# Kernel optimization log

Hardware: AMD Instinct MI355X
Metric: run time of the kernel (lower is better)

## Reference

```python
import jax, jax.numpy as jnp
import numpy as np

B, L, D, H = 2, 2048, 2048, 16
HD = D // H          # head dim = 128
R = int(HD * 0.25)   # rotary ndims = 32
SCALE = HD ** -0.5


def _neox_cos_sin(dim, seq_len, base=10000):
    inv_freq = 1.0 / (base ** (jnp.arange(0, dim, 2, dtype=jnp.float32) / dim))
    t = jnp.arange(seq_len, dtype=jnp.float32)
    freqs = jnp.einsum('i,j->ij', t, inv_freq)      # [L, dim/2]
    emb = jnp.concatenate((freqs, freqs), axis=-1)  # [L, dim]
    return emb[None, None].astype(jnp.float32)      # angle cache [1,1,L,dim]


def setup_inputs() -> dict:
    key = jax.random.key(0)
    ks = jax.random.split(key, 5)
    emb = _neox_cos_sin(R, L)
    s = 0.02
    return {
        'x_BLD': jax.random.normal(ks[0], (B, L, D), jnp.float32),
        'cos': jnp.cos(emb),
        'sin': jnp.sin(emb),
        'Wqkv': jax.random.normal(ks[1], (D, 3 * D), jnp.float32) * s,
        'bqkv': jax.random.normal(ks[2], (3 * D,), jnp.float32) * s,
        'Wd': jax.random.normal(ks[3], (D, D), jnp.float32) * s,
        'bd': jax.random.normal(ks[4], (D,), jnp.float32) * s,
    }


def _rotate_half(x):
    x1, x2 = x[..., : x.shape[-1] // 2], x[..., x.shape[-1] // 2 :]
    return jnp.concatenate((-x2, x1), axis=-1)


def reference(x_BLD, cos, sin, Wqkv, bqkv, Wd, bd):
    bsz, seq_len, _ = x_BLD.shape
    qkv = x_BLD @ Wqkv + bqkv                       # [B,L,3D]
    qkv = qkv.reshape(bsz, seq_len, H, 3 * HD)      # per-head interleaved q|k|v
    q = jnp.transpose(qkv[..., :HD], (0, 2, 1, 3))          # [B,H,L,d]
    k = jnp.transpose(qkv[..., HD:2 * HD], (0, 2, 1, 3))
    v = jnp.transpose(qkv[..., 2 * HD:], (0, 2, 1, 3))

    c = cos[:, :, :seq_len, :]
    s = sin[:, :, :seq_len, :]
    q_rot, q_pass = q[..., :R], q[..., R:]
    k_rot, k_pass = k[..., :R], k[..., R:]
    q_rot = q_rot * c + _rotate_half(q_rot) * s
    k_rot = k_rot * c + _rotate_half(k_rot) * s
    q = jnp.concatenate((q_rot, q_pass), axis=-1)
    k = jnp.concatenate((k_rot, k_pass), axis=-1)

    scores = jnp.einsum('bhqd,bhkd->bhqk', q, k) * SCALE    # [B,H,L,L]
    causal = jnp.tril(jnp.ones((seq_len, seq_len), bool))
    scores = jnp.where(causal, scores, jnp.finfo(scores.dtype).min)
    attn = jax.nn.softmax(scores, axis=-1)
    out = jnp.einsum('bhqk,bhkd->bhqd', attn, v)            # [B,H,L,d]
    out = jnp.transpose(out, (0, 2, 1, 3)).reshape(bsz, seq_len, D)
    return out @ Wd + bd
```

## Files before the change

### kernel.cpp

```cpp
#include <hip/hip_runtime.h>
#include <cstdint>


namespace {

constexpr int B_ = 2, L_ = 2048, D_ = 2048, H_ = 16, HD_ = 128, R_ = 32;
constexpr float SCALE_ = 0.08838834764831845f;

typedef _Float16 f16;
typedef __attribute__((ext_vector_type(8))) _Float16 f16x8;
typedef __attribute__((ext_vector_type(4))) _Float16 f16x4;
typedef __attribute__((ext_vector_type(8))) unsigned short u16x8;
typedef __attribute__((ext_vector_type(4))) float    f32x4;

__device__ __forceinline__ void gload_lds16(const void* g, void* l) {
    __builtin_amdgcn_global_load_lds(
        (const __attribute__((address_space(1))) void*)g,
        (__attribute__((address_space(3))) void*)l, 16, 0, 0);
}

__global__ __launch_bounds__(256) void cast_x_k(const float* __restrict__ x,
                                                f16* __restrict__ xh)
{
    const size_t i = ((size_t)blockIdx.x * 256 + threadIdx.x) * 4;
    const float4 v = *(const float4*)&x[i];
    f16x4 h; h[0] = (f16)v.x; h[1] = (f16)v.y; h[2] = (f16)v.z; h[3] = (f16)v.w;
    *(f16x4*)&xh[i] = h;
}

template <int KIND>
__global__ __launch_bounds__(256) void transW_k(const float* __restrict__ W,
                                                f16* __restrict__ WT)
{
    const int t = threadIdx.x;
    const int n0 = blockIdx.x * 32, k0 = blockIdx.y * 32;
    const int stride = (KIND == 0) ? 2048 : 6144;
    const int c0 = (KIND == 0) ? n0 : ((n0 >> 7) * 384 + (KIND - 1) * 128 + (n0 & 127));

    __shared__ float tl[32][33];

    const int kr = t >> 3, cc = (t & 7) * 4;
    const float4 v = *(const float4*)&W[(size_t)(k0 + kr) * stride + c0 + cc];
    tl[kr][cc + 0] = v.x; tl[kr][cc + 1] = v.y;
    tl[kr][cc + 2] = v.z; tl[kr][cc + 3] = v.w;
    __syncthreads();

    const int nr = t >> 3, kk = (t & 7) * 4;
    f16x4 w;
    w[0] = (f16)tl[kk + 0][nr]; w[1] = (f16)tl[kk + 1][nr];
    w[2] = (f16)tl[kk + 2][nr]; w[3] = (f16)tl[kk + 3][nr];
    *(f16x4*)&WT[(size_t)(n0 + nr) * 2048 + k0 + kk] = w;
}

template <int MODE>
__global__ __launch_bounds__(256) void hgemm_k(
    const f16* __restrict__ A, const f16* __restrict__ Bt,
    const float* __restrict__ bias, void* __restrict__ C)
{
    const int tid  = threadIdx.x;
    const int lane = tid & 63;
    const int wid  = tid >> 6;
    const int n0 = blockIdx.x * 128, m0 = blockIdx.y * 128;
    const int wm = (wid >> 1) * 64, wn = (wid & 1) * 64;

    __shared__ uint4 ldsb[1024];
    char* AsB = (char*)ldsb;
    char* BsB = AsB + 8192;

    int gOffA[2], gOffB[2];
    char *ldsA[2], *ldsB[2];
    #pragma unroll
    for (int i = 0; i < 2; ++i) {
        const int j = 2 * wid + i;
        const int t = j * 64 + lane;
        const int m  = t >> 2;
        const int kc = (t & 3) ^ ((t >> 3) & 3);
        gOffA[i] = (m0 + m) * 2048 + kc * 8;
        gOffB[i] = (n0 + m) * 2048 + kc * 8;
        ldsA[i] = AsB + j * 1024;
        ldsB[i] = BsB + j * 1024;
    }

    const int rowa = wm + (lane & 15);
    const int rowb = wn + (lane & 15);
    const int aBase = rowa * 64 + (((lane >> 4) ^ ((rowa >> 1) & 3)) << 4);
    const int bBase = rowb * 64 + (((lane >> 4) ^ ((rowb >> 1) & 3)) << 4);

    f32x4 acc[4][4];
    #pragma unroll
    for (int i = 0; i < 4; ++i)
        #pragma unroll
        for (int j = 0; j < 4; ++j)
            acc[i][j] = (f32x4){0.f, 0.f, 0.f, 0.f};

    for (int k0 = 0; k0 < 2048; k0 += 32) {
        __syncthreads();
        #pragma unroll
        for (int i = 0; i < 2; ++i) {
            gload_lds16(A  + (size_t)gOffA[i] + k0, ldsA[i]);
            gload_lds16(Bt + (size_t)gOffB[i] + k0, ldsB[i]);
        }
        __syncthreads();

        f16x8 af[4], bf[4];
        #pragma unroll
        for (int mf = 0; mf < 4; ++mf) af[mf] = *(const f16x8*)(AsB + aBase + mf * 1024);
        #pragma unroll
        for (int nf = 0; nf < 4; ++nf) bf[nf] = *(const f16x8*)(BsB + bBase + nf * 1024);
        #pragma unroll
        for (int mf = 0; mf < 4; ++mf)
            #pragma unroll
            for (int nf = 0; nf < 4; ++nf)
                acc[mf][nf] = __builtin_amdgcn_mfma_f32_16x16x32_f16(
                    af[mf], bf[nf], acc[mf][nf], 0, 0, 0);
    }

    #pragma unroll
    for (int nf = 0; nf < 4; ++nf) {
        const int col = n0 + wn + nf * 16 + (lane & 15);
        float bn;
        if (MODE == 0) bn = bias[col];
        else           bn = bias[(col >> 7) * 384 + (MODE - 1) * 128 + (col & 127)];
        #pragma unroll
        for (int mf = 0; mf < 4; ++mf) {
            const int rbase = m0 + wm + mf * 16 + ((lane >> 4) << 2);
            #pragma unroll
            for (int r = 0; r < 4; ++r) {
                const float v = acc[mf][nf][r] + bn;
                const int m = rbase + r;
                if (MODE == 0) {
                    ((float*)C)[(size_t)m * 2048 + col] = v;
                } else {
                    const int b = m >> 11, l = m & (L_ - 1);
                    const int h = col >> 7, d = col & 127;
                    ((f16*)C)[((size_t)(b * H_ + h) * L_ + l) * HD_ + d] = (f16)v;
                }
            }
        }
    }
}

__global__ __launch_bounds__(256) void rope_k(
    f16* __restrict__ Qp, f16* __restrict__ Kp,
    const float* __restrict__ cosp, const float* __restrict__ sinp)
{
    const int idx = blockIdx.x * 256 + threadIdx.x;
    const int j = idx & 15;
    const int bhl = idx >> 4;
    const int l = bhl & (L_ - 1);
    const float c = cosp[l * R_ + j];
    const float s = sinp[l * R_ + j];
    f16* qp = Qp + (size_t)bhl * HD_;
    f16* kp = Kp + (size_t)bhl * HD_;
    const float q1 = (float)qp[j], q2 = (float)qp[j + 16];
    qp[j]      = (f16)(q1 * c - q2 * s);
    qp[j + 16] = (f16)(q2 * c + q1 * s);
    const float k1 = (float)kp[j], k2 = (float)kp[j + 16];
    kp[j]      = (f16)(k1 * c - k2 * s);
    kp[j + 16] = (f16)(k2 * c + k1 * s);
}

__global__ __launch_bounds__(256) void attn2_k(
    const f16* __restrict__ Qh, const f16* __restrict__ Kh,
    const f16* __restrict__ Vh, f16* __restrict__ Oh)
{
    const int tid  = threadIdx.x;
    const int lane = tid & 63;
    const int wid  = tid >> 6;
    const int qtb  = blockIdx.x;
    const int bh   = blockIdx.y;
    const int lr   = lane >> 4;
    const int lc   = lane & 15;
    const int l7   = lane & 7;

    __shared__ f16 Ksh[64 * 128];
    __shared__ f16 Vts[128 * 64];
    __shared__ f16 Pls[4][16 * 64];

    const f16* Qb = Qh + (size_t)bh * (L_ * HD_);
    const f16* Kb = Kh + (size_t)bh * (L_ * HD_);
    const f16* Vb = Vh + (size_t)bh * (L_ * HD_);
    char* const KshB = (char*)Ksh;
    char* const VtsB = (char*)Vts;
    char* const PwB  = (char*)(&Pls[wid][0]);

    #pragma unroll
    for (int ph = 0; ph < 2; ++ph) {
        const int qe  = ph ? (31 - qtb) : qtb;
        const int q0  = qe * 64;
        const int wq0 = q0 + wid * 16;

        f16x8 qa[4];
        #pragma unroll
        for (int j = 0; j < 4; ++j)
            qa[j] = *(const f16x8*)&Qb[(size_t)(wq0 + lc) * HD_ + j * 32 + lr * 8];

        f32x4 of[8];
        #pragma unroll
        for (int ds = 0; ds < 8; ++ds) of[ds] = (f32x4){0.f, 0.f, 0.f, 0.f};
        float m_run[4] = {-1e30f, -1e30f, -1e30f, -1e30f};
        float l_run[4] = {0.f, 0.f, 0.f, 0.f};

        const int nkv = qe + 1;
        for (int t = 0; t < nkv; ++t) {
            const int k0 = t * 64;
            __syncthreads();
            #pragma unroll
            for (int i = 0; i < 4; ++i) {
                const int slot = i * 256 + tid;
                const int row = slot >> 4, cch = slot & 15;
                const f16* src = Kb + (size_t)(k0 + row) * HD_ + (cch ^ (row & 7)) * 8;
                char* dst = KshB + (i * 256 + wid * 64) * 16;
                gload_lds16(src, dst);
            }
            #pragma unroll
            for (int rnd = 0; rnd < 2; ++rnd) {
                const int pc = rnd * 256 + tid;
                const int kp = pc & 31, dc = pc >> 5;
                const f16x8 va = *(const f16x8*)&Vb[(size_t)(k0 + 2 * kp) * HD_ + dc * 8];
                const f16x8 vb2 = *(const f16x8*)&Vb[(size_t)(k0 + 2 * kp + 1) * HD_ + dc * 8];
                const u16x8 au = *(const u16x8*)&va;
                const u16x8 bu = *(const u16x8*)&vb2;
                #pragma unroll
                for (int i = 0; i < 8; ++i) {
                    const int d = dc * 8 + i;
                    const unsigned int pv = (unsigned)au[i] | ((unsigned)bu[i] << 16);
                    *(unsigned int*)(VtsB + d * 128 + ((4 * kp) ^ ((d & 7) << 4))) = pv;
                }
            }
            __syncthreads();

            f32x4 sacc[4];
            #pragma unroll
            for (int ks = 0; ks < 4; ++ks) sacc[ks] = (f32x4){0.f, 0.f, 0.f, 0.f};
            #pragma unroll
            for (int ks = 0; ks < 4; ++ks) {
                const int rowk = ks * 16 + lc;
                f16x8 kb[4];
                #pragma unroll
                for (int j = 0; j < 4; ++j)
                    kb[j] = *(const f16x8*)(KshB + rowk * 256 + (((j * 4 + lr) ^ l7) * 16));
                #pragma unroll
                for (int j = 0; j < 4; ++j)
                    sacc[ks] = __builtin_amdgcn_mfma_f32_16x16x32_f16(
                        qa[j], kb[j], sacc[ks], 0, 0, 0);
            }
            #pragma unroll
            for (int ks = 0; ks < 4; ++ks)
                #pragma unroll
                for (int r = 0; r < 4; ++r) sacc[ks][r] *= SCALE_;
            if (t == qe) {
                #pragma unroll
                for (int ks = 0; ks < 4; ++ks)
                    #pragma unroll
                    for (int r = 0; r < 4; ++r)
                        if (k0 + ks * 16 + lc > wq0 + lr * 4 + r) sacc[ks][r] = -1e30f;
            }
            float mx[4];
            #pragma unroll
            for (int r = 0; r < 4; ++r)
                mx[r] = fmaxf(fmaxf(sacc[0][r], sacc[1][r]),
                              fmaxf(sacc[2][r], sacc[3][r]));
            #pragma unroll
            for (int msk = 1; msk <= 8; msk <<= 1)
                #pragma unroll
                for (int r = 0; r < 4; ++r)
                    mx[r] = fmaxf(mx[r], __shfl_xor(mx[r], msk));
            float alpha[4];
            #pragma unroll
            for (int r = 0; r < 4; ++r) {
                mx[r] = fmaxf(mx[r], m_run[r]);
                alpha[r] = __expf(m_run[r] - mx[r]);
                m_run[r] = mx[r];
            }
            float ls[4] = {0.f, 0.f, 0.f, 0.f};
            #pragma unroll
            for (int ks = 0; ks < 4; ++ks)
                #pragma unroll
                for (int r = 0; r < 4; ++r) {
                    const float p = __expf(sacc[ks][r] - m_run[r]);
                    ls[r] += p;
                    sacc[ks][r] = p;
                }
            #pragma unroll
            for (int ks = 0; ks < 4; ++ks)
                #pragma unroll
                for (int r = 0; r < 4; ++r) {
                    const int q = lr * 4 + r;
                    *(f16*)(PwB + q * 128 + ((ks * 32 + lc * 2) ^ ((q & 7) << 4))) =
                        (f16)sacc[ks][r];
                }
            #pragma unroll
            for (int msk = 1; msk <= 8; msk <<= 1)
                #pragma unroll
                for (int r = 0; r < 4; ++r) ls[r] += __shfl_xor(ls[r], msk);
            #pragma unroll
            for (int r = 0; r < 4; ++r) l_run[r] = l_run[r] * alpha[r] + ls[r];
            #pragma unroll
            for (int ds = 0; ds < 8; ++ds)
                #pragma unroll
                for (int r = 0; r < 4; ++r) of[ds][r] *= alpha[r];

            f16x8 pa[2];
            #pragma unroll
            for (int kc = 0; kc < 2; ++kc)
                pa[kc] = *(const f16x8*)(PwB + lc * 128 +
                         ((lr * 16 + kc * 64) ^ ((lc & 7) << 4)));
            #pragma unroll
            for (int ds = 0; ds < 8; ++ds) {
                const int d = ds * 16 + lc;
                #pragma unroll
                for (int kc = 0; kc < 2; ++kc) {
                    const f16x8 vb = *(const f16x8*)(VtsB + d * 128 +
                                     ((lr * 16 + kc * 64) ^ ((d & 7) << 4)));
                    of[ds] = __builtin_amdgcn_mfma_f32_16x16x32_f16(
                        pa[kc], vb, of[ds], 0, 0, 0);
                }
            }
        }

        const int b = bh >> 4, h = bh & (H_ - 1);
        #pragma unroll
        for (int r = 0; r < 4; ++r) {
            const int q = wq0 + lr * 4 + r;
            const float inv = 1.0f / l_run[r];
            f16* orow = Oh + ((size_t)(b * L_ + q)) * D_ + h * HD_;
            #pragma unroll
            for (int ds = 0; ds < 8; ++ds)
                orow[ds * 16 + lc] = (f16)(of[ds][r] * inv);
        }
    }
}

}

extern "C" void kernel_launch(void* const* d_in, const int* in_sizes, int n_in,
                              void* d_out, int out_size, void* d_ws, size_t ws_size,
                              hipStream_t stream)
{
    (void)in_sizes; (void)n_in; (void)out_size; (void)ws_size;

    const float* x    = (const float*)d_in[0];
    const float* cosp = (const float*)d_in[1];
    const float* sinp = (const float*)d_in[2];
    const float* Wqkv = (const float*)d_in[3];
    const float* bqkv = (const float*)d_in[4];
    const float* Wd   = (const float*)d_in[5];
    const float* bd   = (const float*)d_in[6];
    float* out = (float*)d_out;

    const size_t SZ = (size_t)B_ * H_ * L_ * HD_;
    f16* Qh = (f16*)d_ws;
    f16* Kh = Qh + SZ;
    f16* Vh = Kh + SZ;
    f16* xh = Vh + SZ;
    f16* Oh = xh;
    f16* WT = xh + SZ;

    const dim3 gT(64, 64), gG(16, 32);

    cast_x_k<<<8192, 256, 0, stream>>>(x, xh);

    transW_k<1><<<gT, 256, 0, stream>>>(Wqkv, WT);
    hgemm_k<1><<<gG, 256, 0, stream>>>(xh, WT, bqkv, Qh);
    transW_k<2><<<gT, 256, 0, stream>>>(Wqkv, WT);
    hgemm_k<2><<<gG, 256, 0, stream>>>(xh, WT, bqkv, Kh);
    transW_k<3><<<gT, 256, 0, stream>>>(Wqkv, WT);
    hgemm_k<3><<<gG, 256, 0, stream>>>(xh, WT, bqkv, Vh);

    rope_k<<<4096, 256, 0, stream>>>(Qh, Kh, cosp, sinp);

    attn2_k<<<dim3(16, 32), 256, 0, stream>>>(Qh, Kh, Vh, Oh);

    transW_k<0><<<gT, 256, 0, stream>>>(Wd, WT);
    hgemm_k<0><<<gG, 256, 0, stream>>>(Oh, WT, bd, out);
}
```

Measured before the change: 438.2 us.

## Fuse QKV projection into one GEMM and restructure attention grid and softmax layout

The three separate weight-transpose and GEMM launches for Q, K and V become a single transpose of the full Wqkv and one 48x32-block GEMM, whose epilogue routes each column to Q, K or V. The attention kernel no longer pairs two query tiles per block. It launches one block per query tile (32x32 grid, longest tiles first) and computes S transposed (K as the A operand), so row max and sum reductions need only two cross-lane shuffles, and P is written with vectorized f16x4 stores. This removes launch overhead and raises GEMM parallelism. The cost is per-block load imbalance in attention and extra shuffles to broadcast alpha and l.

```diff
diff --git a/kernel.cpp b/kernel.cpp
--- a/kernel.cpp
+++ b/kernel.cpp
@@ -28,19 +28,17 @@
     *(f16x4*)&xh[i] = h;
 }
 
-template <int KIND>
+template <int STRIDE>
 __global__ __launch_bounds__(256) void transW_k(const float* __restrict__ W,
                                                 f16* __restrict__ WT)
 {
     const int t = threadIdx.x;
     const int n0 = blockIdx.x * 32, k0 = blockIdx.y * 32;
-    const int stride = (KIND == 0) ? 2048 : 6144;
-    const int c0 = (KIND == 0) ? n0 : ((n0 >> 7) * 384 + (KIND - 1) * 128 + (n0 & 127));
 
     __shared__ float tl[32][33];
 
     const int kr = t >> 3, cc = (t & 7) * 4;
-    const float4 v = *(const float4*)&W[(size_t)(k0 + kr) * stride + c0 + cc];
+    const float4 v = *(const float4*)&W[(size_t)(k0 + kr) * STRIDE + n0 + cc];
     tl[kr][cc + 0] = v.x; tl[kr][cc + 1] = v.y;
     tl[kr][cc + 2] = v.z; tl[kr][cc + 3] = v.w;
     __syncthreads();
@@ -55,7 +53,8 @@
 template <int MODE>
 __global__ __launch_bounds__(256) void hgemm_k(
     const f16* __restrict__ A, const f16* __restrict__ Bt,
-    const float* __restrict__ bias, void* __restrict__ C)
+    const float* __restrict__ bias, float* __restrict__ Cf,
+    f16* __restrict__ Qp, f16* __restrict__ Kp, f16* __restrict__ Vp)
 {
     const int tid  = threadIdx.x;
     const int lane = tid & 63;
@@ -118,9 +117,7 @@
     #pragma unroll
     for (int nf = 0; nf < 4; ++nf) {
         const int col = n0 + wn + nf * 16 + (lane & 15);
-        float bn;
-        if (MODE == 0) bn = bias[col];
-        else           bn = bias[(col >> 7) * 384 + (MODE - 1) * 128 + (col & 127)];
+        const float bn = bias[col];
         #pragma unroll
         for (int mf = 0; mf < 4; ++mf) {
             const int rbase = m0 + wm + mf * 16 + ((lane >> 4) << 2);
@@ -129,11 +126,14 @@
                 const float v = acc[mf][nf][r] + bn;
                 const int m = rbase + r;
                 if (MODE == 0) {
-                    ((float*)C)[(size_t)m * 2048 + col] = v;
+                    Cf[(size_t)m * 2048 + col] = v;
                 } else {
                     const int b = m >> 11, l = m & (L_ - 1);
-                    const int h = col >> 7, d = col & 127;
-                    ((f16*)C)[((size_t)(b * H_ + h) * L_ + l) * HD_ + d] = (f16)v;
+                    const int hseg = col / 384;
+                    const int rr = col - hseg * 384;
+                    const int sel = rr >> 7, d = rr & 127;
+                    f16* dst = (sel == 0) ? Qp : (sel == 1) ? Kp : Vp;
+                    dst[((size_t)(b * H_ + hseg) * L_ + l) * HD_ + d] = (f16)v;
                 }
             }
         }
@@ -160,14 +160,14 @@
     kp[j + 16] = (f16)(k2 * c + k1 * s);
 }
 
-__global__ __launch_bounds__(256) void attn2_k(
+__global__ __launch_bounds__(256) void attn3_k(
     const f16* __restrict__ Qh, const f16* __restrict__ Kh,
     const f16* __restrict__ Vh, f16* __restrict__ Oh)
 {
     const int tid  = threadIdx.x;
     const int lane = tid & 63;
     const int wid  = tid >> 6;
-    const int qtb  = blockIdx.x;
+    const int qe   = 31 - (int)blockIdx.x;
     const int bh   = blockIdx.y;
     const int lr   = lane >> 4;
     const int lc   = lane & 15;
@@ -184,151 +184,141 @@
     char* const VtsB = (char*)Vts;
     char* const PwB  = (char*)(&Pls[wid][0]);
 
-    #pragma unroll
-    for (int ph = 0; ph < 2; ++ph) {
-        const int qe  = ph ? (31 - qtb) : qtb;
-        const int q0  = qe * 64;
-        const int wq0 = q0 + wid * 16;
-
-        f16x8 qa[4];
-        #pragma unroll
-        for (int j = 0; j < 4; ++j)
-            qa[j] = *(const f16x8*)&Qb[(size_t)(wq0 + lc) * HD_ + j * 32 + lr * 8];
-
-        f32x4 of[8];
-        #pragma unroll
-        for (int ds = 0; ds < 8; ++ds) of[ds] = (f32x4){0.f, 0.f, 0.f, 0.f};
-        float m_run[4] = {-1e30f, -1e30f, -1e30f, -1e30f};
-        float l_run[4] = {0.f, 0.f, 0.f, 0.f};
-
-        const int nkv = qe + 1;
-        for (int t = 0; t < nkv; ++t) {
-            const int k0 = t * 64;
-            __syncthreads();
-            #pragma unroll
-            for (int i = 0; i < 4; ++i) {
-                const int slot = i * 256 + tid;
-                const int row = slot >> 4, cch = slot & 15;
-                const f16* src = Kb + (size_t)(k0 + row) * HD_ + (cch ^ (row & 7)) * 8;
-                char* dst = KshB + (i * 256 + wid * 64) * 16;
-                gload_lds16(src, dst);
+    const int q0  = qe * 64;
+    const int wq0 = q0 + wid * 16;
+
+    f16x8 qa[4];
+    #pragma unroll
+    for (int j = 0; j < 4; ++j)
+        qa[j] = *(const f16x8*)&Qb[(size_t)(wq0 + lc) * HD_ + j * 32 + lr * 8];
+
+    f32x4 of[8];
+    #pragma unroll
+    for (int ds = 0; ds < 8; ++ds) of[ds] = (f32x4){0.f, 0.f, 0.f, 0.f};
+    float m_run = -1e30f, l_run = 0.f;
+
+    for (int t = 0; t <= qe; ++t) {
+        const int k0 = t * 64;
+        __syncthreads();
+        #pragma unroll
+        for (int i = 0; i < 4; ++i) {
+            const int slot = i * 256 + tid;
+            const int row = slot >> 4, cch = slot & 15;
+            const f16* src = Kb + (size_t)(k0 + row) * HD_ + (cch ^ (row & 7)) * 8;
+            char* dst = KshB + (i * 256 + wid * 64) * 16;
+            gload_lds16(src, dst);
+        }
+        #pragma unroll
+        for (int rnd = 0; rnd < 2; ++rnd) {
+            const int pc = rnd * 256 + tid;
+            const int kp = pc & 31, dc = pc >> 5;
+            const f16x8 va  = *(const f16x8*)&Vb[(size_t)(k0 + 2 * kp) * HD_ + dc * 8];
+            const f16x8 vb2 = *(const f16x8*)&Vb[(size_t)(k0 + 2 * kp + 1) * HD_ + dc * 8];
+            const u16x8 au = *(const u16x8*)&va;
+            const u16x8 bu = *(const u16x8*)&vb2;
+            #pragma unroll
+            for (int i = 0; i < 8; ++i) {
+                const int d = dc * 8 + i;
+                const unsigned int pv = (unsigned)au[i] | ((unsigned)bu[i] << 16);
+                *(unsigned int*)(VtsB + d * 128 + ((4 * kp) ^ ((d & 7) << 4))) = pv;
             }
-            #pragma unroll
-            for (int rnd = 0; rnd < 2; ++rnd) {
-                const int pc = rnd * 256 + tid;
-                const int kp = pc & 31, dc = pc >> 5;
-                const f16x8 va = *(const f16x8*)&Vb[(size_t)(k0 + 2 * kp) * HD_ + dc * 8];
-                const f16x8 vb2 = *(const f16x8*)&Vb[(size_t)(k0 + 2 * kp + 1) * HD_ + dc * 8];
-                const u16x8 au = *(const u16x8*)&va;
-                const u16x8 bu = *(const u16x8*)&vb2;
-                #pragma unroll
-                for (int i = 0; i < 8; ++i) {
-                    const int d = dc * 8 + i;
-                    const unsigned int pv = (unsigned)au[i] | ((unsigned)bu[i] << 16);
-                    *(unsigned int*)(VtsB + d * 128 + ((4 * kp) ^ ((d & 7) << 4))) = pv;
-                }
-            }
-            __syncthreads();
-
-            f32x4 sacc[4];
-            #pragma unroll
-            for (int ks = 0; ks < 4; ++ks) sacc[ks] = (f32x4){0.f, 0.f, 0.f, 0.f};
-            #pragma unroll
-            for (int ks = 0; ks < 4; ++ks) {
-                const int rowk = ks * 16 + lc;
-                f16x8 kb[4];
-                #pragma unroll
-                for (int j = 0; j < 4; ++j)
-                    kb[j] = *(const f16x8*)(KshB + rowk * 256 + (((j * 4 + lr) ^ l7) * 16));
-                #pragma unroll
-                for (int j = 0; j < 4; ++j)
-                    sacc[ks] = __builtin_amdgcn_mfma_f32_16x16x32_f16(
-                        qa[j], kb[j], sacc[ks], 0, 0, 0);
-            }
+        }
+        __syncthreads();
+
+        f32x4 sacc[4];
+        #pragma unroll
+        for (int ks = 0; ks < 4; ++ks) sacc[ks] = (f32x4){0.f, 0.f, 0.f, 0.f};
+        #pragma unroll
+        for (int ks = 0; ks < 4; ++ks) {
+            const int rowk = ks * 16 + lc;
+            f16x8 kb[4];
+            #pragma unroll
+            for (int j = 0; j < 4; ++j)
+                kb[j] = *(const f16x8*)(KshB + rowk * 256 + (((j * 4 + lr) ^ l7) * 16));
+            #pragma unroll
+            for (int j = 0; j < 4; ++j)
+                sacc[ks] = __builtin_amdgcn_mfma_f32_16x16x32_f16(
+                    kb[j], qa[j], sacc[ks], 0, 0, 0);
+        }
+        #pragma unroll
+        for (int ks = 0; ks < 4; ++ks)
+            #pragma unroll
+            for (int r = 0; r < 4; ++r) sacc[ks][r] *= SCALE_;
+        if (t == qe) {
             #pragma unroll
             for (int ks = 0; ks < 4; ++ks)
                 #pragma unroll
-                for (int r = 0; r < 4; ++r) sacc[ks][r] *= SCALE_;
-            if (t == qe) {
-                #pragma unroll
-                for (int ks = 0; ks < 4; ++ks)
-                    #pragma unroll
-                    for (int r = 0; r < 4; ++r)
-                        if (k0 + ks * 16 + lc > wq0 + lr * 4 + r) sacc[ks][r] = -1e30f;
+                for (int r = 0; r < 4; ++r)
+                    if (k0 + ks * 16 + lr * 4 + r > wq0 + lc) sacc[ks][r] = -1e30f;
+        }
+
+        float mx = sacc[0][0];
+        #pragma unroll
+        for (int ks = 0; ks < 4; ++ks)
+            #pragma unroll
+            for (int r = 0; r < 4; ++r) mx = fmaxf(mx, sacc[ks][r]);
+        mx = fmaxf(mx, __shfl_xor(mx, 16));
+        mx = fmaxf(mx, __shfl_xor(mx, 32));
+        mx = fmaxf(mx, m_run);
+        const float alpha = __expf(m_run - mx);
+        m_run = mx;
+        float ls = 0.f;
+        #pragma unroll
+        for (int ks = 0; ks < 4; ++ks)
+            #pragma unroll
+            for (int r = 0; r < 4; ++r) {
+                const float p = __expf(sacc[ks][r] - mx);
+                ls += p;
+                sacc[ks][r] = p;
             }
-            float mx[4];
-            #pragma unroll
-            for (int r = 0; r < 4; ++r)
-                mx[r] = fmaxf(fmaxf(sacc[0][r], sacc[1][r]),
-                              fmaxf(sacc[2][r], sacc[3][r]));
-            #pragma unroll
-            for (int msk = 1; msk <= 8; msk <<= 1)
-                #pragma unroll
-                for (int r = 0; r < 4; ++r)
-                    mx[r] = fmaxf(mx[r], __shfl_xor(mx[r], msk));
-            float alpha[4];
-            #pragma unroll
-            for (int r = 0; r < 4; ++r) {
-                mx[r] = fmaxf(mx[r], m_run[r]);
-                alpha[r] = __expf(m_run[r] - mx[r]);
-                m_run[r] = mx[r];
+        #pragma unroll
+        for (int ks = 0; ks < 4; ++ks) {
+            f16x4 h4;
+            h4[0] = (f16)sacc[ks][0]; h4[1] = (f16)sacc[ks][1];
+            h4[2] = (f16)sacc[ks][2]; h4[3] = (f16)sacc[ks][3];
+            *(f16x4*)(PwB + lc * 128 + ((ks * 32 + lr * 8) ^ ((lc & 7) << 4))) = h4;
+        }
+        ls += __shfl_xor(ls, 16);
+        ls += __shfl_xor(ls, 32);
+        l_run = l_run * alpha + ls;
+        float af4[4];
+        #pragma unroll
+        for (int r = 0; r < 4; ++r) af4[r] = __shfl(alpha, lr * 4 + r);
+        #pragma unroll
+        for (int ds = 0; ds < 8; ++ds)
+            #pragma unroll
+            for (int r = 0; r < 4; ++r) of[ds][r] *= af4[r];
+
+        f16x8 pa[2];
+        #pragma unroll
+        for (int kc = 0; kc < 2; ++kc)
+            pa[kc] = *(const f16x8*)(PwB + lc * 128 +
+                     ((lr * 16 + kc * 64) ^ ((lc & 7) << 4)));
+        #pragma unroll
+        for (int ds = 0; ds < 8; ++ds) {
+            const int d = ds * 16 + lc;
+            #pragma unroll
+            for (int kc = 0; kc < 2; ++kc) {
+                const f16x8 vb = *(const f16x8*)(VtsB + d * 128 +
+                                 ((lr * 16 + kc * 64) ^ ((d & 7) << 4)));
+                of[ds] = __builtin_amdgcn_mfma_f32_16x16x32_f16(
+                    pa[kc], vb, of[ds], 0, 0, 0);
             }
-            float ls[4] = {0.f, 0.f, 0.f, 0.f};
-            #pragma unroll
-            for (int ks = 0; ks < 4; ++ks)
-                #pragma unroll
-                for (int r = 0; r < 4; ++r) {
-                    const float p = __expf(sacc[ks][r] - m_run[r]);
-                    ls[r] += p;
-                    sacc[ks][r] = p;
-                }
-            #pragma unroll
-            for (int ks = 0; ks < 4; ++ks)
-                #pragma unroll
-                for (int r = 0; r < 4; ++r) {
-                    const int q = lr * 4 + r;
-                    *(f16*)(PwB + q * 128 + ((ks * 32 + lc * 2) ^ ((q & 7) << 4))) =
-                        (f16)sacc[ks][r];
-                }
-            #pragma unroll
-            for (int msk = 1; msk <= 8; msk <<= 1)
-                #pragma unroll
-                for (int r = 0; r < 4; ++r) ls[r] += __shfl_xor(ls[r], msk);
-            #pragma unroll
-            for (int r = 0; r < 4; ++r) l_run[r] = l_run[r] * alpha[r] + ls[r];
-            #pragma unroll
-            for (int ds = 0; ds < 8; ++ds)
-                #pragma unroll
-                for (int r = 0; r < 4; ++r) of[ds][r] *= alpha[r];
-
-            f16x8 pa[2];
-            #pragma unroll
-            for (int kc = 0; kc < 2; ++kc)
-                pa[kc] = *(const f16x8*)(PwB + lc * 128 +
-                         ((lr * 16 + kc * 64) ^ ((lc & 7) << 4)));
-            #pragma unroll
-            for (int ds = 0; ds < 8; ++ds) {
-                const int d = ds * 16 + lc;
-                #pragma unroll
-                for (int kc = 0; kc < 2; ++kc) {
-                    const f16x8 vb = *(const f16x8*)(VtsB + d * 128 +
-                                     ((lr * 16 + kc * 64) ^ ((d & 7) << 4)));
-                    of[ds] = __builtin_amdgcn_mfma_f32_16x16x32_f16(
-                        pa[kc], vb, of[ds], 0, 0, 0);
-                }
-            }
-        }
-
-        const int b = bh >> 4, h = bh & (H_ - 1);
-        #pragma unroll
-        for (int r = 0; r < 4; ++r) {
-            const int q = wq0 + lr * 4 + r;
-            const float inv = 1.0f / l_run[r];
-            f16* orow = Oh + ((size_t)(b * L_ + q)) * D_ + h * HD_;
-            #pragma unroll
-            for (int ds = 0; ds < 8; ++ds)
-                orow[ds * 16 + lc] = (f16)(of[ds][r] * inv);
-        }
+        }
+    }
+
+    const int b = bh >> 4, h = bh & (H_ - 1);
+    float li[4];
+    #pragma unroll
+    for (int r = 0; r < 4; ++r) li[r] = __shfl(l_run, lr * 4 + r);
+    #pragma unroll
+    for (int r = 0; r < 4; ++r) {
+        const int q = wq0 + lr * 4 + r;
+        const float inv = 1.0f / li[r];
+        f16* orow = Oh + ((size_t)(b * L_ + q)) * D_ + h * HD_;
+        #pragma unroll
+        for (int ds = 0; ds < 8; ++ds)
+            orow[ds * 16 + lc] = (f16)(of[ds][r] * inv);
     }
 }
 
@@ -357,21 +347,15 @@
     f16* Oh = xh;
     f16* WT = xh + SZ;
 
-    const dim3 gT(64, 64), gG(16, 32);
-
     cast_x_k<<<8192, 256, 0, stream>>>(x, xh);
 
-    transW_k<1><<<gT, 256, 0, stream>>>(Wqkv, WT);
-    hgemm_k<1><<<gG, 256, 0, stream>>>(xh, WT, bqkv, Qh);
-    transW_k<2><<<gT, 256, 0, stream>>>(Wqkv, WT);
-    hgemm_k<2><<<gG, 256, 0, stream>>>(xh, WT, bqkv, Kh);
-    transW_k<3><<<gT, 256, 0, stream>>>(Wqkv, WT);
-    hgemm_k<3><<<gG, 256, 0, stream>>>(xh, WT, bqkv, Vh);
+    transW_k<6144><<<dim3(192, 64), 256, 0, stream>>>(Wqkv, WT);
+    hgemm_k<1><<<dim3(48, 32), 256, 0, stream>>>(xh, WT, bqkv, nullptr, Qh, Kh, Vh);
 
     rope_k<<<4096, 256, 0, stream>>>(Qh, Kh, cosp, sinp);
 
-    attn2_k<<<dim3(16, 32), 256, 0, stream>>>(Qh, Kh, Vh, Oh);
-
-    transW_k<0><<<gT, 256, 0, stream>>>(Wd, WT);
-    hgemm_k<0><<<gG, 256, 0, stream>>>(Oh, WT, bd, out);
-}
+    attn3_k<<<dim3(32, 32), 256, 0, stream>>>(Qh, Kh, Vh, Oh);
+
+    transW_k<2048><<<dim3(64, 64), 256, 0, stream>>>(Wd, WT);
+    hgemm_k<0><<<dim3(16, 32), 256, 0, stream>>>(Oh, WT, bd, out, nullptr, nullptr, nullptr);
+}
```

Measured after the change: 483.4 us. 10.3% more time.
